# Optimization experiments

Measured on AMD Instinct MI355X. Metric: run time of the kernel, lower is better.

Reference implementation:

```python
import jax, jax.numpy as jnp
import numpy as np

D_HEAD = 128
N_HEADS = 8
BATCH = 8
SEQ = 1024


def setup_inputs() -> dict:
    key = jax.random.key(0)
    ks = jax.random.split(key, 11)
    d, nh = D_HEAD, N_HEADS
    D = nh * d
    s_in = 1.0 / np.sqrt(d)   # torch Linear default init bound, fan_in=d
    s_out = 1.0 / np.sqrt(D)  # fan_in=D for out_proj
    u = lambda k, shape, s: jax.random.uniform(k, shape, jnp.float32, -s, s)
    return {
        "q": jax.random.normal(ks[0], (BATCH, SEQ, d), jnp.float32),
        "k": jax.random.normal(ks[1], (BATCH, SEQ, d), jnp.float32),
        "v": jax.random.normal(ks[2], (BATCH, SEQ, d), jnp.float32),
        "Wq": u(ks[3], (d, D), s_in), "bq": u(ks[4], (D,), s_in),
        "Wk": u(ks[5], (d, D), s_in), "bk": u(ks[6], (D,), s_in),
        "Wv": u(ks[7], (d, D), s_in), "bv": u(ks[8], (D,), s_in),
        "Wo": u(ks[9], (D, d), s_out), "bo": u(ks[10], (d,), s_out),
    }


def reference(q, k, v, Wq, bq, Wk, bk, Wv, bv, Wo, bo):
    B, T, d_in = q.shape
    S = k.shape[1]
    nh = N_HEADS
    # projections: [B, L, nh*d] -> [B, nh, L, d]
    split = lambda x: x.reshape(x.shape[0], x.shape[1], nh, -1).transpose(0, 2, 1, 3)
    qh = split(q @ Wq + bq)
    kh = split(k @ Wk + bk)
    vh = split(v @ Wv + bv)
    d_head = qh.shape[-1]
    # scaled dot-product scores: [B, nh, T, S]
    scores = jnp.einsum('bhtd,bhsd->bhts', qh, kh) / jnp.sqrt(jnp.float32(d_head))
    # causal mask (future positions -> -inf), matches triu(fill(-inf), 1)
    causal = jnp.triu(jnp.ones((T, S), dtype=bool), 1)
    scores = jnp.where(causal[None, None], -jnp.inf, scores)
    # softmax in float32 then cast back, as the original does
    probs = jax.nn.softmax(scores.astype(jnp.float32), axis=-1).astype(scores.dtype)
    o = jnp.einsum('bhts,bhsd->bhtd', probs, vh)          # [B, nh, T, d]
    o = o.transpose(0, 2, 1, 3).reshape(B, T, nh * d_head)  # [B, T, D]
    return o @ Wo + bo                                     # [B, T, d]
```

## Files before the change

### kernel.cpp

```cpp
#include <hip/hip_runtime.h>
#include <hip/hip_bf16.h>


typedef __attribute__((ext_vector_type(8))) short short8;
typedef __attribute__((ext_vector_type(4))) short short4v;
typedef __attribute__((ext_vector_type(4))) float f32x4;

#define B_   8
#define S_   1024
#define DH_  128
#define NH_  8
#define DM_  1024

#define MFMA16(a, b, c) __builtin_amdgcn_mfma_f32_16x16x32_bf16((a), (b), (c), 0, 0, 0)

#define GLOAD_LDS16(gsrc, ldst)                                              \
  __builtin_amdgcn_global_load_lds(                                          \
      (const __attribute__((address_space(1))) void*)(gsrc),                 \
      (__attribute__((address_space(3))) void*)(ldst), 16, 0, 0)

__device__ __forceinline__ float bf2f(unsigned short u) {
  union { unsigned int i; float f; } x; x.i = ((unsigned int)u) << 16; return x.f;
}
__device__ __forceinline__ unsigned short f2bf(float f) {
  union { float f; unsigned int i; } x; x.f = f;
  unsigned int r = (x.i + 0x7fffu + ((x.i >> 16) & 1u)) >> 16;
  return (unsigned short)r;
}
__device__ __forceinline__ unsigned short f2h(float f) {
  union { _Float16 h; unsigned short u; } x; x.h = (_Float16)f; return x.u;
}
__device__ __forceinline__ float h2f(unsigned short u) {
  union { unsigned short u; _Float16 h; } x; x.u = u; return (float)x.h;
}
__device__ __forceinline__ float ldany(const void* p, int i, int fp) {
  return fp ? ((const float*)p)[i] : bf2f(((const unsigned short*)p)[i]);
}

__global__ void k_detect(const unsigned short* __restrict__ in, int* __restrict__ flag) {
  __shared__ int f;
  int tid = threadIdx.x;
  if (tid == 0) f = 0;
  __syncthreads();
  int t = 0;
  for (int i = tid; i < 16384; i += 256) {
    unsigned h = in[i];
    unsigned e = (h >> 7) & 0xFFu, m = h & 0x7Fu;
    if (e == 0xFFu || (e == 0u && m != 0u)) t = 1;
  }
  if (t) atomicOr(&f, 1);
  __syncthreads();
  if (tid == 0) *flag = f;
}

__global__ void k_cvt_x(const void* __restrict__ q, const void* __restrict__ k,
                        const void* __restrict__ v, const int* __restrict__ flag,
                        unsigned short* __restrict__ Xq, unsigned short* __restrict__ Xk,
                        unsigned short* __restrict__ Xv) {
  const int fp = *flag;
  int z = blockIdx.y;
  const void* in = (z == 0) ? q : (z == 1) ? k : v;
  unsigned short* out = (z == 0) ? Xq : (z == 1) ? Xk : Xv;
  int e4 = (blockIdx.x * 256 + threadIdx.x) * 4;
  if (fp) {
    f32x4 x = *(const f32x4*)&((const float*)in)[e4];
    short4v o;
#pragma unroll
    for (int j = 0; j < 4; ++j) o[j] = (short)f2bf(x[j]);
    *(short4v*)&out[e4] = o;
  } else {
    *(short4v*)&out[e4] = *(const short4v*)&((const unsigned short*)in)[e4];
  }
}

__global__ void k_cvt_w(const void* __restrict__ Wq, const void* __restrict__ Wk,
                        const void* __restrict__ Wv, const void* __restrict__ Wo,
                        const void* __restrict__ bq, const void* __restrict__ bk,
                        const void* __restrict__ bv, const void* __restrict__ bo,
                        const int* __restrict__ flag,
                        unsigned short* __restrict__ wqT, unsigned short* __restrict__ wkT,
                        unsigned short* __restrict__ wvT, unsigned short* __restrict__ woT,
                        unsigned short* __restrict__ bqc, unsigned short* __restrict__ bkc,
                        unsigned short* __restrict__ bvc, unsigned short* __restrict__ boc) {
  const int fp = *flag;
  int g = blockIdx.x * 256 + threadIdx.x;
  if (g < 393216) {
    int z = g >> 17, e = g & 131071;
    const void* in = (z == 0) ? Wq : (z == 1) ? Wk : Wv;
    unsigned short* out = (z == 0) ? wqT : (z == 1) ? wkT : wvT;
    int r = e >> 10, c = e & 1023;
    out[c * 128 + r] = f2bf(ldany(in, e, fp));
  } else if (g < 524288) {
    int e = g - 393216;
    int r = e >> 7, c = e & 127;
    woT[c * 1024 + r] = f2bf(ldany(Wo, e, fp));
  } else if (g < 525312) {
    int e = g - 524288; bqc[e] = f2bf(ldany(bq, e, fp));
  } else if (g < 526336) {
    int e = g - 525312; bkc[e] = f2bf(ldany(bk, e, fp));
  } else if (g < 527360) {
    int e = g - 526336; bvc[e] = f2bf(ldany(bv, e, fp));
  } else if (g < 527488) {
    int e = g - 527360; boc[e] = f2bf(ldany(bo, e, fp));
  }
}

__global__ __launch_bounds__(256) void k_qkv(
    const unsigned short* __restrict__ Xq, const unsigned short* __restrict__ Xk,
    const unsigned short* __restrict__ Xv,
    const unsigned short* __restrict__ WqT, const unsigned short* __restrict__ WkT,
    const unsigned short* __restrict__ WvT,
    const unsigned short* __restrict__ bq, const unsigned short* __restrict__ bk,
    const unsigned short* __restrict__ bv,
    unsigned short* __restrict__ Qp, unsigned short* __restrict__ Kp,
    unsigned short* __restrict__ VpT) {
  __shared__ __align__(16) unsigned short vtile[128][136];

  const int mat = blockIdx.z;
  const unsigned short* X    = (mat == 0) ? Xq  : (mat == 1) ? Xk  : Xv;
  const unsigned short* WT   = (mat == 0) ? WqT : (mat == 1) ? WkT : WvT;
  const unsigned short* bias = (mat == 0) ? bq  : (mat == 1) ? bk  : bv;
  const float scale = (mat == 0) ? (1.4426950408889634f / 11.313708498984761f) : 1.0f;

  const int tid = threadIdx.x, lane = tid & 63, wave = tid >> 6;
  const int wm = wave >> 1, wn = wave & 1;
  const int l15 = lane & 15, lg = lane >> 4;
  const int mbase = blockIdx.x * 128 + wm * 64;
  const int nbase = blockIdx.y * 128 + wn * 64;

  short8 a[4][4];
#pragma unroll
  for (int mi = 0; mi < 4; ++mi)
#pragma unroll
    for (int kk = 0; kk < 4; ++kk)
      a[mi][kk] = *(const short8*)&X[(mbase + mi * 16 + l15) * DH_ + kk * 32 + lg * 8];

  f32x4 acc[4][4];
#pragma unroll
  for (int mi = 0; mi < 4; ++mi)
#pragma unroll
    for (int ni = 0; ni < 4; ++ni) acc[mi][ni] = (f32x4){0.f, 0.f, 0.f, 0.f};

  short8 bfr[2][4];
#pragma unroll
  for (int kk = 0; kk < 4; ++kk)
    bfr[0][kk] = *(const short8*)&WT[(nbase + l15) * DH_ + kk * 32 + lg * 8];

#pragma unroll
  for (int ni = 0; ni < 4; ++ni) {
    if (ni < 3) {
#pragma unroll
      for (int kk = 0; kk < 4; ++kk)
        bfr[(ni + 1) & 1][kk] =
            *(const short8*)&WT[(nbase + (ni + 1) * 16 + l15) * DH_ + kk * 32 + lg * 8];
    }
#pragma unroll
    for (int mi = 0; mi < 4; ++mi)
#pragma unroll
      for (int kk = 0; kk < 4; ++kk)
        acc[mi][ni] = MFMA16(a[mi][kk], bfr[ni & 1][kk], acc[mi][ni]);
  }

#pragma unroll
  for (int mi = 0; mi < 4; ++mi)
#pragma unroll
    for (int ni = 0; ni < 4; ++ni) {
      int nl = wn * 64 + ni * 16 + l15;
      float bv_ = bf2f(bias[blockIdx.y * 128 + nl]);
#pragma unroll
      for (int reg = 0; reg < 4; ++reg) {
        int ml_ = wm * 64 + mi * 16 + lg * 4 + reg;
        vtile[ml_][nl] = f2bf((acc[mi][ni][reg] + bv_) * scale);
      }
    }
  __syncthreads();

  const int b = blockIdx.x >> 3;
  const int h = blockIdx.y;
  if (mat < 2) {
    unsigned short* Out = ((mat == 0) ? Qp : Kp) +
        ((b * NH_ + h) * S_ + (blockIdx.x & 7) * 128) * DH_;
#pragma unroll
    for (int j = 0; j < 8; ++j) {
      int r = j * 16 + (tid >> 4);
      int c0 = (tid & 15) * 8;
      short8 v = *(const short8*)&vtile[r][c0];
      *(short8*)&Out[j * 2048 + tid * 8] = v;
    }
  } else {
    int n = tid >> 1;
    int thalf = (tid & 1) * 64;
    int base = ((b * NH_ + h) * DH_ + n) * S_ + (blockIdx.x & 7) * 128 + thalf;
#pragma unroll
    for (int jj = 0; jj < 8; ++jj) {
      short8 v;
#pragma unroll
      for (int j2 = 0; j2 < 8; ++j2) v[j2] = (short)vtile[thalf + jj * 8 + j2][n];
      *(short8*)&VpT[base + jj * 8] = v;
    }
  }
}

__global__ __launch_bounds__(256) void k_attn_split(
    const unsigned short* __restrict__ Qp, const unsigned short* __restrict__ Kp,
    const unsigned short* __restrict__ VpT,
    unsigned short* __restrict__ Opart, float* __restrict__ ml,
    unsigned short* __restrict__ O) {
  __shared__ __align__(16) unsigned short kbuf[2][4096];
  __shared__ __align__(16) unsigned short vbuf[2][4096];
  __shared__ __align__(16) unsigned short plds[4][16][48];

  const int tid = threadIdx.x, lane = tid & 63, w = tid >> 6;
  const int l15 = lane & 15, lg = lane >> 4;

  const int bid = blockIdx.x;
  const int swz = (bid & 7) * 320 + (bid >> 3);
  const int bh = swz / 40;
  const int bj = 39 - (swz % 40);
  int G, c;
  if (bj < 4)       { G = bj;                  c = 0; }
  else if (bj < 12) { G = 4 + ((bj - 4) >> 1); c = (bj - 4) & 1; }
  else if (bj < 24) { G = 8 + (bj - 12) / 3;   c = (bj - 12) % 3; }
  else              { G = 12 + ((bj - 24) >> 2); c = (bj - 24) & 3; }
  const int qw = 4 * G + w;
  const int q0 = qw * 16;
  const int cd = G >> 2;
  const bool dia = (c == cd);
  const int sbeg = c * 256;
  const int nt_w   = dia ? ((qw >> 1) + 1 - 8 * c) : 8;
  const int nt_blk = dia ? (2 * G + 2 - 8 * c) : 8;

  const unsigned short* Qb = Qp + bh * (S_ * DH_);
  const unsigned short* Kb = Kp + bh * (S_ * DH_);
  const unsigned short* Vb = VpT + bh * (DH_ * S_);

  const int krow4 = lane >> 4;
  const int kslot = lane & 15;
  const int vd16  = lane >> 2;
  const int vslot = lane & 3;

#define STAGE(bb, sb_) do {                                                        \
    int r0_ = w * 8 + krow4;                                                       \
    GLOAD_LDS16(Kb + ((sb_) + r0_) * DH_ + ((kslot ^ (r0_ & 7)) * 8),              \
                &kbuf[bb][(w * 8) * 128]);                                         \
    int r1_ = w * 8 + 4 + krow4;                                                   \
    GLOAD_LDS16(Kb + ((sb_) + r1_) * DH_ + ((kslot ^ (r1_ & 7)) * 8),              \
                &kbuf[bb][(w * 8 + 4) * 128]);                                     \
    int d0_ = w * 32 + vd16;                                                       \
    GLOAD_LDS16(Vb + d0_ * S_ + (sb_) + vslot * 8, &vbuf[bb][(w * 32) * 32]);      \
    int d1_ = w * 32 + 16 + vd16;                                                  \
    GLOAD_LDS16(Vb + d1_ * S_ + (sb_) + vslot * 8, &vbuf[bb][(w * 32 + 16) * 32]); \
  } while (0)

  short8 qf[4];
#pragma unroll
  for (int kk = 0; kk < 4; ++kk)
    qf[kk] = *(const short8*)&Qb[(q0 + l15) * DH_ + kk * 32 + lg * 8];

  short8 ones;
#pragma unroll
  for (int jj = 0; jj < 8; ++jj) ones[jj] = (short)0x3F80;

  f32x4 of[8], l_acc;
  float m_[4];
#pragma unroll
  for (int di = 0; di < 8; ++di) of[di] = (f32x4){0.f, 0.f, 0.f, 0.f};
  l_acc = (f32x4){0.f, 0.f, 0.f, 0.f};
#pragma unroll
  for (int reg = 0; reg < 4; ++reg) m_[reg] = -1e30f;

  STAGE(0, sbeg);
  __syncthreads();

  for (int kt = 0; kt < nt_blk; ++kt) {
    const int cb = kt & 1;
    if (kt + 1 < nt_blk) STAGE(cb ^ 1, sbeg + (kt + 1) * 32);

    if (kt < nt_w) {
      const int sb = sbeg + kt * 32;
      const int xsl = l15 & 7;

      f32x4 s0 = (f32x4){0.f, 0.f, 0.f, 0.f}, s1 = (f32x4){0.f, 0.f, 0.f, 0.f};
      __builtin_amdgcn_s_setprio(1);
#pragma unroll
      for (int kk = 0; kk < 4; ++kk) {
        short8 kf0 = *(const short8*)&kbuf[cb][l15 * 128 + (((kk * 4 + lg) ^ xsl) * 8)];
        short8 kf1 = *(const short8*)&kbuf[cb][(16 + l15) * 128 + (((kk * 4 + lg) ^ xsl) * 8)];
        s0 = MFMA16(qf[kk], kf0, s0);
        s1 = MFMA16(qf[kk], kf1, s1);
      }
      __builtin_amdgcn_s_setprio(0);

      if (dia && kt == nt_w - 1) {
        const int qrow = q0 + lg * 4;
#pragma unroll
        for (int reg = 0; reg < 4; ++reg) {
          if (sb + l15 > qrow + reg)      s0[reg] = -1e30f;
          if (sb + 16 + l15 > qrow + reg) s1[reg] = -1e30f;
        }
      }

      bool need = false;
      float vmax[4];
#pragma unroll
      for (int reg = 0; reg < 4; ++reg) {
        vmax[reg] = fmaxf(s0[reg], s1[reg]);
        need |= (vmax[reg] > m_[reg] + 8.0f);
      }
      if (__any(need)) {
        float alpha[4];
#pragma unroll
        for (int reg = 0; reg < 4; ++reg) {
          float rm = vmax[reg];
#pragma unroll
          for (int d = 1; d < 16; d <<= 1) rm = fmaxf(rm, __shfl_xor(rm, d));
          float mn = fmaxf(m_[reg], rm);
          alpha[reg] = __builtin_amdgcn_exp2f(m_[reg] - mn);
          m_[reg] = mn;
        }
#pragma unroll
        for (int di = 0; di < 8; ++di)
#pragma unroll
          for (int reg = 0; reg < 4; ++reg) of[di][reg] *= alpha[reg];
#pragma unroll
        for (int reg = 0; reg < 4; ++reg) l_acc[reg] *= alpha[reg];
      }

#pragma unroll
      for (int reg = 0; reg < 4; ++reg) {
        float p0 = __builtin_amdgcn_exp2f(s0[reg] - m_[reg]);
        float p1 = __builtin_amdgcn_exp2f(s1[reg] - m_[reg]);
        union { float f; unsigned int i; } u0, u1;
        u0.f = p0; u1.f = p1;
        plds[w][lg * 4 + reg][l15]      = (unsigned short)((u0.i + 0x8000u) >> 16);
        plds[w][lg * 4 + reg][16 + l15] = (unsigned short)((u1.i + 0x8000u) >> 16);
      }

      short8 pa = *(const short8*)&plds[w][l15][lg * 8];

      __builtin_amdgcn_s_setprio(1);
#pragma unroll
      for (int di = 0; di < 8; ++di) {
        short8 vfd = *(const short8*)&vbuf[cb][(di * 16 + l15) * 32 + lg * 8];
        of[di] = MFMA16(pa, vfd, of[di]);
      }
      l_acc = MFMA16(pa, ones, l_acc);
      __builtin_amdgcn_s_setprio(0);
    }
    __syncthreads();
  }

  if (qw < 16) {
    const int b = bh >> 3, h = bh & 7;
#pragma unroll
    for (int reg = 0; reg < 4; ++reg) {
      int row = lg * 4 + reg;
      float inv = 1.0f / l_acc[reg];
      int qq = q0 + row;
#pragma unroll
      for (int di = 0; di < 8; ++di)
        O[(b * S_ + qq) * DM_ + h * DH_ + di * 16 + l15] = f2bf(of[di][reg] * inv);
    }
  } else {
    int runit;
    if (qw < 32)      runit = 16 + 2 * (qw - 16) + c;
    else if (qw < 48) runit = 48 + 3 * (qw - 32) + c;
    else              runit = 96 + 4 * (qw - 48) + c;
    const int g = bh * 160 + runit;
    unsigned short* op = Opart + g * 2048;
    float* mlg = ml + g * 32;
#pragma unroll
    for (int reg = 0; reg < 4; ++reg) {
      int row = lg * 4 + reg;
      float inv = 1.0f / l_acc[reg];
#pragma unroll
      for (int di = 0; di < 8; ++di)
        op[row * 128 + di * 16 + l15] = f2h(of[di][reg] * inv);
      if (l15 == 0) {
        mlg[row * 2]     = m_[reg];
        mlg[row * 2 + 1] = l_acc[reg];
      }
    }
  }
#undef STAGE
}

__global__ void k_combine(const unsigned short* __restrict__ Opart,
                          const float* __restrict__ ml,
                          unsigned short* __restrict__ O) {
  const int bh = blockIdx.x / 48, qw = 16 + blockIdx.x % 48;
  const int nc = (qw >> 4) + 1;
  const int rbase = (qw < 32) ? 16 + 2 * (qw - 16)
                  : (qw < 48) ? 48 + 3 * (qw - 32)
                              : 96 + 4 * (qw - 48);
  const int g0 = bh * 160 + rbase;
  const int tid = threadIdx.x;
  const int row = tid >> 4, d0 = (tid & 15) * 8;

  float m[4], l[4];
  float mx = -1e30f;
  for (int i = 0; i < nc; ++i) {
    m[i] = ml[(g0 + i) * 32 + row * 2];
    l[i] = ml[(g0 + i) * 32 + row * 2 + 1];
    mx = fmaxf(mx, m[i]);
  }
  float wt[4], wsum = 0.f;
  for (int i = 0; i < nc; ++i) { wt[i] = l[i] * exp2f(m[i] - mx); wsum += wt[i]; }
  float invw = 1.0f / wsum;

  float acc[8];
#pragma unroll
  for (int jj = 0; jj < 8; ++jj) acc[jj] = 0.f;
  for (int i = 0; i < nc; ++i) {
    short8 v = *(const short8*)&Opart[(g0 + i) * 2048 + row * 128 + d0];
    float wgt = wt[i];
#pragma unroll
    for (int jj = 0; jj < 8; ++jj) acc[jj] += wgt * h2f((unsigned short)v[jj]);
  }

  const int b = bh >> 3, h = bh & 7;
  const int qq = qw * 16 + row;
  short8 o;
#pragma unroll
  for (int jj = 0; jj < 8; ++jj) o[jj] = (short)f2bf(acc[jj] * invw);
  *(short8*)&O[(b * S_ + qq) * DM_ + h * DH_ + d0] = o;
}

__global__ __launch_bounds__(256) void k_attn(
    const unsigned short* __restrict__ Qp, const unsigned short* __restrict__ Kp,
    const unsigned short* __restrict__ VpT, unsigned short* __restrict__ O) {
  __shared__ __align__(16) unsigned short plds[4][2][16][48];

  const int qt = 7 - blockIdx.x;
  const int bh = blockIdx.y;
  const int tid = threadIdx.x, lane = tid & 63, w = tid >> 6;
  const int l15 = lane & 15, lg = lane >> 4;
  const int q0 = qt * 128 + w * 32;

  const unsigned short* Qb = Qp + bh * (S_ * DH_);
  const unsigned short* Kb = Kp + bh * (S_ * DH_);
  const unsigned short* Vb = VpT + bh * (DH_ * S_);

  short8 qf[2][4];
#pragma unroll
  for (int mi = 0; mi < 2; ++mi)
#pragma unroll
    for (int kk = 0; kk < 4; ++kk)
      qf[mi][kk] = *(const short8*)&Qb[(q0 + mi * 16 + l15) * DH_ + kk * 32 + lg * 8];

  f32x4 of[2][8];
  float m_[2][4], l_[2][4];
#pragma unroll
  for (int mi = 0; mi < 2; ++mi) {
#pragma unroll
    for (int di = 0; di < 8; ++di) of[mi][di] = (f32x4){0.f, 0.f, 0.f, 0.f};
#pragma unroll
    for (int reg = 0; reg < 4; ++reg) { m_[mi][reg] = -1e30f; l_[mi][reg] = 0.f; }
  }

  const int ntiles = q0 / 32 + 1;
  for (int kt = 0; kt < ntiles; ++kt) {
    const int sb = kt * 32;
    const bool lastt = (kt == ntiles - 1);

    f32x4 s[2][2];
#pragma unroll
    for (int mi = 0; mi < 2; ++mi)
#pragma unroll
      for (int ni = 0; ni < 2; ++ni) s[mi][ni] = (f32x4){0.f, 0.f, 0.f, 0.f};
#pragma unroll
    for (int ni = 0; ni < 2; ++ni) {
      short8 kf[4];
#pragma unroll
      for (int kk = 0; kk < 4; ++kk)
        kf[kk] = *(const short8*)&Kb[(sb + ni * 16 + l15) * DH_ + kk * 32 + lg * 8];
#pragma unroll
      for (int mi = 0; mi < 2; ++mi)
#pragma unroll
        for (int kk = 0; kk < 4; ++kk)
          s[mi][ni] = MFMA16(qf[mi][kk], kf[kk], s[mi][ni]);
    }

#pragma unroll
    for (int mi = 0; mi < 2; ++mi) {
      float alpha[4];
#pragma unroll
      for (int reg = 0; reg < 4; ++reg) {
        int q = q0 + mi * 16 + lg * 4 + reg;
        float v0 = s[mi][0][reg];
        float v1 = s[mi][1][reg];
        if (lastt) {
          if (sb + l15 > q)      v0 = -1e30f;
          if (sb + 16 + l15 > q) v1 = -1e30f;
        }
        float rmax = fmaxf(v0, v1);
#pragma unroll
        for (int d = 1; d < 16; d <<= 1) rmax = fmaxf(rmax, __shfl_xor(rmax, d));
        float mn = fmaxf(m_[mi][reg], rmax);
        alpha[reg] = __builtin_amdgcn_exp2f(m_[mi][reg] - mn);
        m_[mi][reg] = mn;
        float p0 = __builtin_amdgcn_exp2f(v0 - mn), p1 = __builtin_amdgcn_exp2f(v1 - mn);
        float rs = p0 + p1;
#pragma unroll
        for (int d = 1; d < 16; d <<= 1) rs += __shfl_xor(rs, d);
        l_[mi][reg] = l_[mi][reg] * alpha[reg] + rs;
        plds[w][mi][lg * 4 + reg][l15]      = f2bf(p0);
        plds[w][mi][lg * 4 + reg][16 + l15] = f2bf(p1);
      }
#pragma unroll
      for (int di = 0; di < 8; ++di)
#pragma unroll
        for (int reg = 0; reg < 4; ++reg) of[mi][di][reg] *= alpha[reg];
    }

    short8 pa[2];
#pragma unroll
    for (int mi = 0; mi < 2; ++mi)
      pa[mi] = *(const short8*)&plds[w][mi][l15][lg * 8];

#pragma unroll
    for (int di = 0; di < 8; ++di) {
      short8 vf = *(const short8*)&Vb[(di * 16 + l15) * S_ + sb + lg * 8];
#pragma unroll
      for (int mi = 0; mi < 2; ++mi) of[mi][di] = MFMA16(pa[mi], vf, of[mi][di]);
    }
  }

  const int b = bh >> 3, h = bh & 7;
#pragma unroll
  for (int mi = 0; mi < 2; ++mi)
#pragma unroll
    for (int reg = 0; reg < 4; ++reg) {
      float inv = 1.0f / l_[mi][reg];
      int q = q0 + mi * 16 + lg * 4 + reg;
#pragma unroll
      for (int di = 0; di < 8; ++di) {
        int d = di * 16 + l15;
        O[(b * S_ + q) * DM_ + h * DH_ + d] = f2bf(of[mi][di][reg] * inv);
      }
    }
}

__global__ __launch_bounds__(256) void k_oproj(
    const unsigned short* __restrict__ O, const unsigned short* __restrict__ WoT,
    float* __restrict__ outacc) {
  const int tid = threadIdx.x, lane = tid & 63, wave = tid >> 6;
  const int wm = wave >> 1, wn = wave & 1;
  const int l15 = lane & 15, lg = lane >> 4;
  const int mbase = blockIdx.x * 128 + wm * 64;
  const int kc = blockIdx.y;

  f32x4 acc[4][4];
#pragma unroll
  for (int mi = 0; mi < 4; ++mi)
#pragma unroll
    for (int ni = 0; ni < 4; ++ni) acc[mi][ni] = (f32x4){0.f, 0.f, 0.f, 0.f};

  for (int ks = 0; ks < 8; ++ks) {
    int kb = kc * 256 + ks * 32;
    short8 a[4], bfr[4];
#pragma unroll
    for (int mi = 0; mi < 4; ++mi)
      a[mi] = *(const short8*)&O[(mbase + mi * 16 + l15) * DM_ + kb + lg * 8];
#pragma unroll
    for (int ni = 0; ni < 4; ++ni)
      bfr[ni] = *(const short8*)&WoT[(wn * 64 + ni * 16 + l15) * DM_ + kb + lg * 8];
#pragma unroll
    for (int mi = 0; mi < 4; ++mi)
#pragma unroll
      for (int ni = 0; ni < 4; ++ni) acc[mi][ni] = MFMA16(a[mi], bfr[ni], acc[mi][ni]);
  }

  float* oa = outacc + kc * (8192 * 128);
#pragma unroll
  for (int mi = 0; mi < 4; ++mi)
#pragma unroll
    for (int ni = 0; ni < 4; ++ni) {
      int n = wn * 64 + ni * 16 + l15;
#pragma unroll
      for (int reg = 0; reg < 4; ++reg) {
        int m = mbase + mi * 16 + lg * 4 + reg;
        oa[m * 128 + n] = acc[mi][ni][reg];
      }
    }
}

__global__ void k_final(const float* __restrict__ outacc,
                        const unsigned short* __restrict__ boc,
                        const int* __restrict__ flag, void* __restrict__ out) {
  int i4 = (blockIdx.x * 256 + threadIdx.x) * 4;
  f32x4 v = *(const f32x4*)&outacc[i4];
  v += *(const f32x4*)&outacc[1048576 + i4];
  v += *(const f32x4*)&outacc[2097152 + i4];
  v += *(const f32x4*)&outacc[3145728 + i4];
  int n0 = i4 & 127;
#pragma unroll
  for (int j = 0; j < 4; ++j) v[j] += bf2f(boc[n0 + j]);
  if (*flag) {
    *(f32x4*)&((float*)out)[i4] = v;
  } else {
    short4v o;
#pragma unroll
    for (int j = 0; j < 4; ++j) o[j] = (short)f2bf(v[j]);
    *(short4v*)&((unsigned short*)out)[i4] = o;
  }
}

extern "C" void kernel_launch(void* const* d_in, const int* in_sizes, int n_in,
                              void* d_out, int out_size, void* d_ws, size_t ws_size,
                              hipStream_t stream) {
  const void* q  = d_in[0];
  const void* k  = d_in[1];
  const void* v  = d_in[2];
  const void* Wq = d_in[3];
  const void* bq = d_in[4];
  const void* Wk = d_in[5];
  const void* bk = d_in[6];
  const void* Wv = d_in[7];
  const void* bv = d_in[8];
  const void* Wo = d_in[9];
  const void* bo = d_in[10];

  char* ws = (char*)d_ws;
  int*            flag = (int*)(ws + 0);
  unsigned short* wqT  = (unsigned short*)(ws + 4096);
  unsigned short* wkT  = (unsigned short*)(ws + 266240);
  unsigned short* wvT  = (unsigned short*)(ws + 528384);
  unsigned short* woT  = (unsigned short*)(ws + 790528);
  unsigned short* bqc  = (unsigned short*)(ws + 1052672);
  unsigned short* bkc  = (unsigned short*)(ws + 1054720);
  unsigned short* bvc  = (unsigned short*)(ws + 1056768);
  unsigned short* boc  = (unsigned short*)(ws + 1058816);
  unsigned short* Xq   = (unsigned short*)(ws + 2097152);
  unsigned short* Xk   = (unsigned short*)(ws + 4194304);
  unsigned short* Xv   = (unsigned short*)(ws + 6291456);
  unsigned short* Qp   = (unsigned short*)(ws + 8388608);
  unsigned short* Kp   = (unsigned short*)(ws + 25165824);
  unsigned short* VpT  = (unsigned short*)(ws + 41943040);
  unsigned short* O    = (unsigned short*)(ws + 58720256);
  float*          oacc = (float*)(ws + 75497472);
  unsigned short* Opart= (unsigned short*)(ws + 75497472);
  float*          ml   = (float*)(ws + 2097152);

  const bool use_split = ws_size >= (size_t)117440512;

  k_detect<<<dim3(1), 256, 0, stream>>>((const unsigned short*)q, flag);
  k_cvt_x<<<dim3(1024, 3), 256, 0, stream>>>(q, k, v, flag, Xq, Xk, Xv);
  k_cvt_w<<<dim3(2061), 256, 0, stream>>>(Wq, Wk, Wv, Wo, bq, bk, bv, bo, flag,
                                          wqT, wkT, wvT, woT, bqc, bkc, bvc, boc);
  k_qkv<<<dim3(64, 8, 3), 256, 0, stream>>>(Xq, Xk, Xv, wqT, wkT, wvT, bqc, bkc, bvc,
                                            Qp, Kp, VpT);
  if (use_split) {
    k_attn_split<<<dim3(2560), 256, 0, stream>>>(Qp, Kp, VpT, Opart, ml, O);
    k_combine<<<dim3(3072), 256, 0, stream>>>(Opart, ml, O);
  } else {
    k_attn<<<dim3(8, 64), 256, 0, stream>>>(Qp, Kp, VpT, O);
  }
  k_oproj<<<dim3(64, 4), 256, 0, stream>>>(O, woT, oacc);
  k_final<<<dim3(1024), 256, 0, stream>>>(oacc, boc, flag, d_out);
}
```

Measured before the change: 144.6 us.

## Fuse input conversion into QKV, fuse oproj with bias, swizzle V LDS layout

Removes the separate input-conversion kernel by having the QKV projection load and convert fp32 inputs directly. It replaces the split-K output projection plus the final reduction kernel with a single kernel that does the full K loop over 16-row tiles and writes biased output directly. In the attention kernel it XOR-swizzles the V tile layout in LDS, shrinks the P staging pad from 48 to 44, and drops the s_setprio hints. The aim is fewer launches and less fp32 round-trip traffic, at the cost of a less parallel, less reusing oproj and possible LDS conflict shifts.

```diff
diff --git a/kernel.cpp b/kernel.cpp
--- a/kernel.cpp
+++ b/kernel.cpp
@@ -35,6 +35,18 @@
 }
 __device__ __forceinline__ float ldany(const void* p, int i, int fp) {
   return fp ? ((const float*)p)[i] : bf2f(((const unsigned short*)p)[i]);
+}
+__device__ __forceinline__ short8 ldx8(const void* X, int idx, int fp) {
+  if (fp) {
+    const float* xf = (const float*)X + idx;
+    f32x4 x0 = *(const f32x4*)xf;
+    f32x4 x1 = *(const f32x4*)(xf + 4);
+    short8 o;
+#pragma unroll
+    for (int j = 0; j < 4; ++j) { o[j] = (short)f2bf(x0[j]); o[4 + j] = (short)f2bf(x1[j]); }
+    return o;
+  }
+  return *(const short8*)((const unsigned short*)X + idx);
 }
 
 __global__ void k_detect(const unsigned short* __restrict__ in, int* __restrict__ flag) {
@@ -51,26 +63,6 @@
   if (t) atomicOr(&f, 1);
   __syncthreads();
   if (tid == 0) *flag = f;
-}
-
-__global__ void k_cvt_x(const void* __restrict__ q, const void* __restrict__ k,
-                        const void* __restrict__ v, const int* __restrict__ flag,
-                        unsigned short* __restrict__ Xq, unsigned short* __restrict__ Xk,
-                        unsigned short* __restrict__ Xv) {
-  const int fp = *flag;
-  int z = blockIdx.y;
-  const void* in = (z == 0) ? q : (z == 1) ? k : v;
-  unsigned short* out = (z == 0) ? Xq : (z == 1) ? Xk : Xv;
-  int e4 = (blockIdx.x * 256 + threadIdx.x) * 4;
-  if (fp) {
-    f32x4 x = *(const f32x4*)&((const float*)in)[e4];
-    short4v o;
-#pragma unroll
-    for (int j = 0; j < 4; ++j) o[j] = (short)f2bf(x[j]);
-    *(short4v*)&out[e4] = o;
-  } else {
-    *(short4v*)&out[e4] = *(const short4v*)&((const unsigned short*)in)[e4];
-  }
 }
 
 __global__ void k_cvt_w(const void* __restrict__ Wq, const void* __restrict__ Wk,
@@ -106,18 +98,18 @@
 }
 
 __global__ __launch_bounds__(256) void k_qkv(
-    const unsigned short* __restrict__ Xq, const unsigned short* __restrict__ Xk,
-    const unsigned short* __restrict__ Xv,
+    const void* __restrict__ Xq, const void* __restrict__ Xk, const void* __restrict__ Xv,
     const unsigned short* __restrict__ WqT, const unsigned short* __restrict__ WkT,
     const unsigned short* __restrict__ WvT,
     const unsigned short* __restrict__ bq, const unsigned short* __restrict__ bk,
-    const unsigned short* __restrict__ bv,
+    const unsigned short* __restrict__ bv, const int* __restrict__ flag,
     unsigned short* __restrict__ Qp, unsigned short* __restrict__ Kp,
     unsigned short* __restrict__ VpT) {
   __shared__ __align__(16) unsigned short vtile[128][136];
 
+  const int fp = *flag;
   const int mat = blockIdx.z;
-  const unsigned short* X    = (mat == 0) ? Xq  : (mat == 1) ? Xk  : Xv;
+  const void* X = (mat == 0) ? Xq : (mat == 1) ? Xk : Xv;
   const unsigned short* WT   = (mat == 0) ? WqT : (mat == 1) ? WkT : WvT;
   const unsigned short* bias = (mat == 0) ? bq  : (mat == 1) ? bk  : bv;
   const float scale = (mat == 0) ? (1.4426950408889634f / 11.313708498984761f) : 1.0f;
@@ -133,7 +125,7 @@
   for (int mi = 0; mi < 4; ++mi)
 #pragma unroll
     for (int kk = 0; kk < 4; ++kk)
-      a[mi][kk] = *(const short8*)&X[(mbase + mi * 16 + l15) * DH_ + kk * 32 + lg * 8];
+      a[mi][kk] = ldx8(X, (mbase + mi * 16 + l15) * DH_ + kk * 32 + lg * 8, fp);
 
   f32x4 acc[4][4];
 #pragma unroll
@@ -208,7 +200,7 @@
     unsigned short* __restrict__ O) {
   __shared__ __align__(16) unsigned short kbuf[2][4096];
   __shared__ __align__(16) unsigned short vbuf[2][4096];
-  __shared__ __align__(16) unsigned short plds[4][16][48];
+  __shared__ __align__(16) unsigned short plds[4][16][44];
 
   const int tid = threadIdx.x, lane = tid & 63, w = tid >> 6;
   const int l15 = lane & 15, lg = lane >> 4;
@@ -238,6 +230,7 @@
   const int kslot = lane & 15;
   const int vd16  = lane >> 2;
   const int vslot = lane & 3;
+  const int vsw   = vslot ^ ((vd16 >> 1) & 3);
 
 #define STAGE(bb, sb_) do {                                                        \
     int r0_ = w * 8 + krow4;                                                       \
@@ -247,9 +240,9 @@
     GLOAD_LDS16(Kb + ((sb_) + r1_) * DH_ + ((kslot ^ (r1_ & 7)) * 8),              \
                 &kbuf[bb][(w * 8 + 4) * 128]);                                     \
     int d0_ = w * 32 + vd16;                                                       \
-    GLOAD_LDS16(Vb + d0_ * S_ + (sb_) + vslot * 8, &vbuf[bb][(w * 32) * 32]);      \
+    GLOAD_LDS16(Vb + d0_ * S_ + (sb_) + vsw * 8, &vbuf[bb][(w * 32) * 32]);        \
     int d1_ = w * 32 + 16 + vd16;                                                  \
-    GLOAD_LDS16(Vb + d1_ * S_ + (sb_) + vslot * 8, &vbuf[bb][(w * 32 + 16) * 32]); \
+    GLOAD_LDS16(Vb + d1_ * S_ + (sb_) + vsw * 8, &vbuf[bb][(w * 32 + 16) * 32]);   \
   } while (0)
 
   short8 qf[4];
@@ -272,6 +265,7 @@
   STAGE(0, sbeg);
   __syncthreads();
 
+  const int vrd = lg ^ ((l15 >> 1) & 3);
   for (int kt = 0; kt < nt_blk; ++kt) {
     const int cb = kt & 1;
     if (kt + 1 < nt_blk) STAGE(cb ^ 1, sbeg + (kt + 1) * 32);
@@ -281,7 +275,6 @@
       const int xsl = l15 & 7;
 
       f32x4 s0 = (f32x4){0.f, 0.f, 0.f, 0.f}, s1 = (f32x4){0.f, 0.f, 0.f, 0.f};
-      __builtin_amdgcn_s_setprio(1);
 #pragma unroll
       for (int kk = 0; kk < 4; ++kk) {
         short8 kf0 = *(const short8*)&kbuf[cb][l15 * 128 + (((kk * 4 + lg) ^ xsl) * 8)];
@@ -289,7 +282,6 @@
         s0 = MFMA16(qf[kk], kf0, s0);
         s1 = MFMA16(qf[kk], kf1, s1);
       }
-      __builtin_amdgcn_s_setprio(0);
 
       if (dia && kt == nt_w - 1) {
         const int qrow = q0 + lg * 4;
@@ -338,14 +330,12 @@
 
       short8 pa = *(const short8*)&plds[w][l15][lg * 8];
 
-      __builtin_amdgcn_s_setprio(1);
 #pragma unroll
       for (int di = 0; di < 8; ++di) {
-        short8 vfd = *(const short8*)&vbuf[cb][(di * 16 + l15) * 32 + lg * 8];
+        short8 vfd = *(const short8*)&vbuf[cb][(di * 16 + l15) * 32 + vrd * 8];
         of[di] = MFMA16(pa, vfd, of[di]);
       }
       l_acc = MFMA16(pa, ones, l_acc);
-      __builtin_amdgcn_s_setprio(0);
     }
     __syncthreads();
   }
@@ -429,7 +419,7 @@
 __global__ __launch_bounds__(256) void k_attn(
     const unsigned short* __restrict__ Qp, const unsigned short* __restrict__ Kp,
     const unsigned short* __restrict__ VpT, unsigned short* __restrict__ O) {
-  __shared__ __align__(16) unsigned short plds[4][2][16][48];
+  __shared__ __align__(16) unsigned short plds[4][2][16][44];
 
   const int qt = 7 - blockIdx.x;
   const int bh = blockIdx.y;
@@ -543,66 +533,37 @@
 
 __global__ __launch_bounds__(256) void k_oproj(
     const unsigned short* __restrict__ O, const unsigned short* __restrict__ WoT,
-    float* __restrict__ outacc) {
-  const int tid = threadIdx.x, lane = tid & 63, wave = tid >> 6;
-  const int wm = wave >> 1, wn = wave & 1;
+    const unsigned short* __restrict__ boc, const int* __restrict__ flag,
+    void* __restrict__ out) {
+  const int tid = threadIdx.x, lane = tid & 63, w = tid >> 6;
   const int l15 = lane & 15, lg = lane >> 4;
-  const int mbase = blockIdx.x * 128 + wm * 64;
-  const int kc = blockIdx.y;
-
-  f32x4 acc[4][4];
-#pragma unroll
-  for (int mi = 0; mi < 4; ++mi)
-#pragma unroll
-    for (int ni = 0; ni < 4; ++ni) acc[mi][ni] = (f32x4){0.f, 0.f, 0.f, 0.f};
-
-  for (int ks = 0; ks < 8; ++ks) {
-    int kb = kc * 256 + ks * 32;
-    short8 a[4], bfr[4];
-#pragma unroll
-    for (int mi = 0; mi < 4; ++mi)
-      a[mi] = *(const short8*)&O[(mbase + mi * 16 + l15) * DM_ + kb + lg * 8];
-#pragma unroll
-    for (int ni = 0; ni < 4; ++ni)
-      bfr[ni] = *(const short8*)&WoT[(wn * 64 + ni * 16 + l15) * DM_ + kb + lg * 8];
-#pragma unroll
-    for (int mi = 0; mi < 4; ++mi)
-#pragma unroll
-      for (int ni = 0; ni < 4; ++ni) acc[mi][ni] = MFMA16(a[mi], bfr[ni], acc[mi][ni]);
-  }
-
-  float* oa = outacc + kc * (8192 * 128);
-#pragma unroll
-  for (int mi = 0; mi < 4; ++mi)
-#pragma unroll
-    for (int ni = 0; ni < 4; ++ni) {
-      int n = wn * 64 + ni * 16 + l15;
-#pragma unroll
-      for (int reg = 0; reg < 4; ++reg) {
-        int m = mbase + mi * 16 + lg * 4 + reg;
-        oa[m * 128 + n] = acc[mi][ni][reg];
-      }
-    }
-}
-
-__global__ void k_final(const float* __restrict__ outacc,
-                        const unsigned short* __restrict__ boc,
-                        const int* __restrict__ flag, void* __restrict__ out) {
-  int i4 = (blockIdx.x * 256 + threadIdx.x) * 4;
-  f32x4 v = *(const f32x4*)&outacc[i4];
-  v += *(const f32x4*)&outacc[1048576 + i4];
-  v += *(const f32x4*)&outacc[2097152 + i4];
-  v += *(const f32x4*)&outacc[3145728 + i4];
-  int n0 = i4 & 127;
-#pragma unroll
-  for (int j = 0; j < 4; ++j) v[j] += bf2f(boc[n0 + j]);
-  if (*flag) {
-    *(f32x4*)&((float*)out)[i4] = v;
-  } else {
-    short4v o;
-#pragma unroll
-    for (int j = 0; j < 4; ++j) o[j] = (short)f2bf(v[j]);
-    *(short4v*)&((unsigned short*)out)[i4] = o;
+  const int mrow = blockIdx.x * 16;
+
+  f32x4 acc[2];
+  acc[0] = (f32x4){0.f, 0.f, 0.f, 0.f};
+  acc[1] = (f32x4){0.f, 0.f, 0.f, 0.f};
+
+  for (int ks = 0; ks < 32; ++ks) {
+    int kb = ks * 32;
+    short8 a  = *(const short8*)&O[(mrow + l15) * DM_ + kb + lg * 8];
+    short8 b0 = *(const short8*)&WoT[(w * 32 + l15) * DM_ + kb + lg * 8];
+    short8 b1 = *(const short8*)&WoT[(w * 32 + 16 + l15) * DM_ + kb + lg * 8];
+    acc[0] = MFMA16(a, b0, acc[0]);
+    acc[1] = MFMA16(a, b1, acc[1]);
+  }
+
+  const int fp = *flag;
+#pragma unroll
+  for (int ni = 0; ni < 2; ++ni) {
+    int n = w * 32 + ni * 16 + l15;
+    float bv_ = bf2f(boc[n]);
+#pragma unroll
+    for (int reg = 0; reg < 4; ++reg) {
+      int m = mrow + lg * 4 + reg;
+      float val = acc[ni][reg] + bv_;
+      if (fp) ((float*)out)[m * 128 + n] = val;
+      else    ((unsigned short*)out)[m * 128 + n] = f2bf(val);
+    }
   }
 }
 
@@ -631,31 +592,25 @@
   unsigned short* bkc  = (unsigned short*)(ws + 1054720);
   unsigned short* bvc  = (unsigned short*)(ws + 1056768);
   unsigned short* boc  = (unsigned short*)(ws + 1058816);
-  unsigned short* Xq   = (unsigned short*)(ws + 2097152);
-  unsigned short* Xk   = (unsigned short*)(ws + 4194304);
-  unsigned short* Xv   = (unsigned short*)(ws + 6291456);
+  float*          ml   = (float*)(ws + 2097152);
   unsigned short* Qp   = (unsigned short*)(ws + 8388608);
   unsigned short* Kp   = (unsigned short*)(ws + 25165824);
   unsigned short* VpT  = (unsigned short*)(ws + 41943040);
   unsigned short* O    = (unsigned short*)(ws + 58720256);
-  float*          oacc = (float*)(ws + 75497472);
   unsigned short* Opart= (unsigned short*)(ws + 75497472);
-  float*          ml   = (float*)(ws + 2097152);
 
   const bool use_split = ws_size >= (size_t)117440512;
 
   k_detect<<<dim3(1), 256, 0, stream>>>((const unsigned short*)q, flag);
-  k_cvt_x<<<dim3(1024, 3), 256, 0, stream>>>(q, k, v, flag, Xq, Xk, Xv);
   k_cvt_w<<<dim3(2061), 256, 0, stream>>>(Wq, Wk, Wv, Wo, bq, bk, bv, bo, flag,
                                           wqT, wkT, wvT, woT, bqc, bkc, bvc, boc);
-  k_qkv<<<dim3(64, 8, 3), 256, 0, stream>>>(Xq, Xk, Xv, wqT, wkT, wvT, bqc, bkc, bvc,
-                                            Qp, Kp, VpT);
+  k_qkv<<<dim3(64, 8, 3), 256, 0, stream>>>(q, k, v, wqT, wkT, wvT, bqc, bkc, bvc,
+                                            flag, Qp, Kp, VpT);
   if (use_split) {
     k_attn_split<<<dim3(2560), 256, 0, stream>>>(Qp, Kp, VpT, Opart, ml, O);
     k_combine<<<dim3(3072), 256, 0, stream>>>(Opart, ml, O);
   } else {
     k_attn<<<dim3(8, 64), 256, 0, stream>>>(Qp, Kp, VpT, O);
   }
-  k_oproj<<<dim3(64, 4), 256, 0, stream>>>(O, woT, oacc);
-  k_final<<<dim3(1024), 256, 0, stream>>>(oacc, boc, flag, d_out);
-}
+  k_oproj<<<dim3(512), 256, 0, stream>>>(O, woT, boc, flag, d_out);
+}
```

New measurement: 155.9 us. 1.08x slower.

## Merge conversion kernels, swizzle V LDS layout, drop setprio, prefetch oproj fragments

Applied to the files above, without the earlier changes.

Combines the input and weight conversion kernels into one launch with 8-element vector conversion, cutting one kernel launch. In the split attention kernel, V tiles are XOR-swizzled in LDS to reduce bank conflicts on fragment reads, the P LDS padding shrinks, and s_setprio hints are removed. The output projection now double-buffers its global fragment loads so the next k-step's loads overlap the current MFMAs, at the cost of more registers.

```diff
diff --git a/kernel.cpp b/kernel.cpp
--- a/kernel.cpp
+++ b/kernel.cpp
@@ -53,37 +53,39 @@
   if (tid == 0) *flag = f;
 }
 
-__global__ void k_cvt_x(const void* __restrict__ q, const void* __restrict__ k,
-                        const void* __restrict__ v, const int* __restrict__ flag,
-                        unsigned short* __restrict__ Xq, unsigned short* __restrict__ Xk,
-                        unsigned short* __restrict__ Xv) {
+__global__ void k_cvt(const void* __restrict__ q, const void* __restrict__ k,
+                      const void* __restrict__ v,
+                      const void* __restrict__ Wq, const void* __restrict__ Wk,
+                      const void* __restrict__ Wv, const void* __restrict__ Wo,
+                      const void* __restrict__ bq, const void* __restrict__ bk,
+                      const void* __restrict__ bv, const void* __restrict__ bo,
+                      const int* __restrict__ flag,
+                      unsigned short* __restrict__ Xq, unsigned short* __restrict__ Xk,
+                      unsigned short* __restrict__ Xv,
+                      unsigned short* __restrict__ wqT, unsigned short* __restrict__ wkT,
+                      unsigned short* __restrict__ wvT, unsigned short* __restrict__ woT,
+                      unsigned short* __restrict__ bqc, unsigned short* __restrict__ bkc,
+                      unsigned short* __restrict__ bvc, unsigned short* __restrict__ boc) {
   const int fp = *flag;
-  int z = blockIdx.y;
-  const void* in = (z == 0) ? q : (z == 1) ? k : v;
-  unsigned short* out = (z == 0) ? Xq : (z == 1) ? Xk : Xv;
-  int e4 = (blockIdx.x * 256 + threadIdx.x) * 4;
-  if (fp) {
-    f32x4 x = *(const f32x4*)&((const float*)in)[e4];
-    short4v o;
-#pragma unroll
-    for (int j = 0; j < 4; ++j) o[j] = (short)f2bf(x[j]);
-    *(short4v*)&out[e4] = o;
-  } else {
-    *(short4v*)&out[e4] = *(const short4v*)&((const unsigned short*)in)[e4];
-  }
-}
-
-__global__ void k_cvt_w(const void* __restrict__ Wq, const void* __restrict__ Wk,
-                        const void* __restrict__ Wv, const void* __restrict__ Wo,
-                        const void* __restrict__ bq, const void* __restrict__ bk,
-                        const void* __restrict__ bv, const void* __restrict__ bo,
-                        const int* __restrict__ flag,
-                        unsigned short* __restrict__ wqT, unsigned short* __restrict__ wkT,
-                        unsigned short* __restrict__ wvT, unsigned short* __restrict__ woT,
-                        unsigned short* __restrict__ bqc, unsigned short* __restrict__ bkc,
-                        unsigned short* __restrict__ bvc, unsigned short* __restrict__ boc) {
-  const int fp = *flag;
-  int g = blockIdx.x * 256 + threadIdx.x;
+  if (blockIdx.x < 1536) {
+    int z = blockIdx.x / 512, blk = blockIdx.x % 512;
+    const void* in = (z == 0) ? q : (z == 1) ? k : v;
+    unsigned short* out = (z == 0) ? Xq : (z == 1) ? Xk : Xv;
+    int e8 = (blk * 256 + threadIdx.x) * 8;
+    if (fp) {
+      const float* xf = (const float*)in + e8;
+      f32x4 x0 = *(const f32x4*)xf;
+      f32x4 x1 = *(const f32x4*)(xf + 4);
+      short8 o;
+#pragma unroll
+      for (int j = 0; j < 4; ++j) { o[j] = (short)f2bf(x0[j]); o[4 + j] = (short)f2bf(x1[j]); }
+      *(short8*)&out[e8] = o;
+    } else {
+      *(short8*)&out[e8] = *(const short8*)((const unsigned short*)in + e8);
+    }
+    return;
+  }
+  int g = (blockIdx.x - 1536) * 256 + threadIdx.x;
   if (g < 393216) {
     int z = g >> 17, e = g & 131071;
     const void* in = (z == 0) ? Wq : (z == 1) ? Wk : Wv;
@@ -208,7 +210,7 @@
     unsigned short* __restrict__ O) {
   __shared__ __align__(16) unsigned short kbuf[2][4096];
   __shared__ __align__(16) unsigned short vbuf[2][4096];
-  __shared__ __align__(16) unsigned short plds[4][16][48];
+  __shared__ __align__(16) unsigned short plds[4][16][44];
 
   const int tid = threadIdx.x, lane = tid & 63, w = tid >> 6;
   const int l15 = lane & 15, lg = lane >> 4;
@@ -238,6 +240,7 @@
   const int kslot = lane & 15;
   const int vd16  = lane >> 2;
   const int vslot = lane & 3;
+  const int vsw   = vslot ^ ((vd16 >> 1) & 3);
 
 #define STAGE(bb, sb_) do {                                                        \
     int r0_ = w * 8 + krow4;                                                       \
@@ -247,9 +250,9 @@
     GLOAD_LDS16(Kb + ((sb_) + r1_) * DH_ + ((kslot ^ (r1_ & 7)) * 8),              \
                 &kbuf[bb][(w * 8 + 4) * 128]);                                     \
     int d0_ = w * 32 + vd16;                                                       \
-    GLOAD_LDS16(Vb + d0_ * S_ + (sb_) + vslot * 8, &vbuf[bb][(w * 32) * 32]);      \
+    GLOAD_LDS16(Vb + d0_ * S_ + (sb_) + vsw * 8, &vbuf[bb][(w * 32) * 32]);        \
     int d1_ = w * 32 + 16 + vd16;                                                  \
-    GLOAD_LDS16(Vb + d1_ * S_ + (sb_) + vslot * 8, &vbuf[bb][(w * 32 + 16) * 32]); \
+    GLOAD_LDS16(Vb + d1_ * S_ + (sb_) + vsw * 8, &vbuf[bb][(w * 32 + 16) * 32]);   \
   } while (0)
 
   short8 qf[4];
@@ -272,6 +275,7 @@
   STAGE(0, sbeg);
   __syncthreads();
 
+  const int vrd = lg ^ ((l15 >> 1) & 3);
   for (int kt = 0; kt < nt_blk; ++kt) {
     const int cb = kt & 1;
     if (kt + 1 < nt_blk) STAGE(cb ^ 1, sbeg + (kt + 1) * 32);
@@ -281,7 +285,6 @@
       const int xsl = l15 & 7;
 
       f32x4 s0 = (f32x4){0.f, 0.f, 0.f, 0.f}, s1 = (f32x4){0.f, 0.f, 0.f, 0.f};
-      __builtin_amdgcn_s_setprio(1);
 #pragma unroll
       for (int kk = 0; kk < 4; ++kk) {
         short8 kf0 = *(const short8*)&kbuf[cb][l15 * 128 + (((kk * 4 + lg) ^ xsl) * 8)];
@@ -289,7 +292,6 @@
         s0 = MFMA16(qf[kk], kf0, s0);
         s1 = MFMA16(qf[kk], kf1, s1);
       }
-      __builtin_amdgcn_s_setprio(0);
 
       if (dia && kt == nt_w - 1) {
         const int qrow = q0 + lg * 4;
@@ -338,14 +340,12 @@
 
       short8 pa = *(const short8*)&plds[w][l15][lg * 8];
 
-      __builtin_amdgcn_s_setprio(1);
 #pragma unroll
       for (int di = 0; di < 8; ++di) {
-        short8 vfd = *(const short8*)&vbuf[cb][(di * 16 + l15) * 32 + lg * 8];
+        short8 vfd = *(const short8*)&vbuf[cb][(di * 16 + l15) * 32 + vrd * 8];
         of[di] = MFMA16(pa, vfd, of[di]);
       }
       l_acc = MFMA16(pa, ones, l_acc);
-      __builtin_amdgcn_s_setprio(0);
     }
     __syncthreads();
   }
@@ -429,7 +429,7 @@
 __global__ __launch_bounds__(256) void k_attn(
     const unsigned short* __restrict__ Qp, const unsigned short* __restrict__ Kp,
     const unsigned short* __restrict__ VpT, unsigned short* __restrict__ O) {
-  __shared__ __align__(16) unsigned short plds[4][2][16][48];
+  __shared__ __align__(16) unsigned short plds[4][2][16][44];
 
   const int qt = 7 - blockIdx.x;
   const int bh = blockIdx.y;
@@ -556,19 +556,34 @@
 #pragma unroll
     for (int ni = 0; ni < 4; ++ni) acc[mi][ni] = (f32x4){0.f, 0.f, 0.f, 0.f};
 
+  short8 a[2][4], bfr[2][4];
+  {
+    int kb = kc * 256;
+#pragma unroll
+    for (int mi = 0; mi < 4; ++mi)
+      a[0][mi] = *(const short8*)&O[(mbase + mi * 16 + l15) * DM_ + kb + lg * 8];
+#pragma unroll
+    for (int ni = 0; ni < 4; ++ni)
+      bfr[0][ni] = *(const short8*)&WoT[(wn * 64 + ni * 16 + l15) * DM_ + kb + lg * 8];
+  }
+
+#pragma unroll
   for (int ks = 0; ks < 8; ++ks) {
-    int kb = kc * 256 + ks * 32;
-    short8 a[4], bfr[4];
+    const int cur = ks & 1;
+    if (ks < 7) {
+      int kb = kc * 256 + (ks + 1) * 32;
+#pragma unroll
+      for (int mi = 0; mi < 4; ++mi)
+        a[cur ^ 1][mi] = *(const short8*)&O[(mbase + mi * 16 + l15) * DM_ + kb + lg * 8];
+#pragma unroll
+      for (int ni = 0; ni < 4; ++ni)
+        bfr[cur ^ 1][ni] = *(const short8*)&WoT[(wn * 64 + ni * 16 + l15) * DM_ + kb + lg * 8];
+    }
 #pragma unroll
     for (int mi = 0; mi < 4; ++mi)
-      a[mi] = *(const short8*)&O[(mbase + mi * 16 + l15) * DM_ + kb + lg * 8];
-#pragma unroll
-    for (int ni = 0; ni < 4; ++ni)
-      bfr[ni] = *(const short8*)&WoT[(wn * 64 + ni * 16 + l15) * DM_ + kb + lg * 8];
-#pragma unroll
-    for (int mi = 0; mi < 4; ++mi)
-#pragma unroll
-      for (int ni = 0; ni < 4; ++ni) acc[mi][ni] = MFMA16(a[mi], bfr[ni], acc[mi][ni]);
+#pragma unroll
+      for (int ni = 0; ni < 4; ++ni)
+        acc[mi][ni] = MFMA16(a[cur][mi], bfr[cur][ni], acc[mi][ni]);
   }
 
   float* oa = outacc + kc * (8192 * 128);
@@ -634,20 +649,20 @@
   unsigned short* Xq   = (unsigned short*)(ws + 2097152);
   unsigned short* Xk   = (unsigned short*)(ws + 4194304);
   unsigned short* Xv   = (unsigned short*)(ws + 6291456);
+  float*          ml   = (float*)(ws + 2097152);
   unsigned short* Qp   = (unsigned short*)(ws + 8388608);
   unsigned short* Kp   = (unsigned short*)(ws + 25165824);
   unsigned short* VpT  = (unsigned short*)(ws + 41943040);
   unsigned short* O    = (unsigned short*)(ws + 58720256);
+  unsigned short* Opart= (unsigned short*)(ws + 75497472);
   float*          oacc = (float*)(ws + 75497472);
-  unsigned short* Opart= (unsigned short*)(ws + 75497472);
-  float*          ml   = (float*)(ws + 2097152);
 
   const bool use_split = ws_size >= (size_t)117440512;
 
   k_detect<<<dim3(1), 256, 0, stream>>>((const unsigned short*)q, flag);
-  k_cvt_x<<<dim3(1024, 3), 256, 0, stream>>>(q, k, v, flag, Xq, Xk, Xv);
-  k_cvt_w<<<dim3(2061), 256, 0, stream>>>(Wq, Wk, Wv, Wo, bq, bk, bv, bo, flag,
-                                          wqT, wkT, wvT, woT, bqc, bkc, bvc, boc);
+  k_cvt<<<dim3(3597), 256, 0, stream>>>(q, k, v, Wq, Wk, Wv, Wo, bq, bk, bv, bo, flag,
+                                        Xq, Xk, Xv, wqT, wkT, wvT, woT,
+                                        bqc, bkc, bvc, boc);
   k_qkv<<<dim3(64, 8, 3), 256, 0, stream>>>(Xq, Xk, Xv, wqT, wkT, wvT, bqc, bkc, bvc,
                                             Qp, Kp, VpT);
   if (use_split) {
```

Result: faster. 140.9 us (-2.5%).
